# Kernel tuning notes

Measured on AMD Instinct MI355X. Metric: run time of the kernel, lower is better.

The kernel has to match this reference:

```python
import jax, jax.numpy as jnp
import numpy as np

TEMPERATURE = 0.5
EPS = 1e-8  # torch CosineSimilarity eps


def setup_inputs() -> dict:
    key = jax.random.key(0)
    k1, k2 = jax.random.split(key)
    zis = jax.random.normal(k1, (65536, 256), dtype=jnp.float32)
    zjs = jax.random.normal(k2, (65536, 256), dtype=jnp.float32)
    # default soft labels: one-hot on the positive (first) logit column
    soft_labels = jnp.zeros((4, 3), dtype=jnp.float32).at[:, 0].set(1.0)
    return {"zis": zis, "zjs": zjs, "soft_labels": soft_labels}


def reference(zis, zjs, soft_labels):
    n, d = zis.shape
    nc = n // 2  # number of chunks of size 2
    zi = zis.reshape(nc, 2, d)
    zj = zjs.reshape(nc, 2, d)
    reps = jnp.concatenate([zj, zi], axis=1)  # (nc, 4, d) = cat([zjs, zis])
    # cosine similarity with eps clamp as in torch.nn.CosineSimilarity
    norm = jnp.maximum(jnp.linalg.norm(reps, axis=-1, keepdims=True), EPS)
    reps_n = reps / norm
    sim = jnp.einsum('nid,njd->nij', reps_n, reps_n)  # (nc, 4, 4)
    # positives: diag(sim, +2) then diag(sim, -2) -> cols [2,3,0,1]
    pos = sim[:, jnp.arange(4), jnp.array([2, 3, 0, 1])]  # (nc, 4)
    # negatives: mask removes main diag and +-2 diagonals -> 2 cols per row
    neg_idx = jnp.array([[1, 3], [0, 2], [1, 3], [0, 2]])  # (4, 2)
    neg = jnp.take_along_axis(sim, neg_idx[None, :, :], axis=2)  # (nc, 4, 2)
    logits = jnp.concatenate([pos[..., None], neg], axis=-1) / TEMPERATURE  # (nc,4,3)
    # criterion: exp-normalize (softmax) then -(log ps * soft_labels).sum()
    logp = jax.nn.log_softmax(logits, axis=-1)
    loss = -(logp * soft_labels[None, :, :]).sum()
    return loss / (2 * n)
```

## Files before the change

### kernel.cpp

```cpp
#include <hip/hip_runtime.h>
#include <math.h>


constexpr int D = 256;

__device__ __forceinline__ float dot4(float4 a, float4 b) {
    return fmaf(a.x, b.x, fmaf(a.y, b.y, fmaf(a.z, b.z, a.w * b.w)));
}

template <int CTRL>
__device__ __forceinline__ float dpp_add(float x) {
    int y = __builtin_amdgcn_update_dpp(0, __float_as_int(x), CTRL, 0xF, 0xF, true);
    return x + __int_as_float(y);
}

__device__ __forceinline__ float red16(float x) {
    x = dpp_add<0xB1>(x);
    x = dpp_add<0x4E>(x);
    x = dpp_add<0x124>(x);
    x = dpp_add<0x128>(x);
    return x;
}

__device__ __forceinline__ float rowloss(float a, float b, float c,
                                         float s0, float s1, float s2) {
    float m = fmaxf(fmaxf(a, b), c);
    float lse = m + __logf(__expf(a - m) + __expf(b - m) + __expf(c - m));
    return s0 * (lse - a) + s1 * (lse - b) + s2 * (lse - c);
}

__global__ __launch_bounds__(256, 4) void ntxent_stage1(
    const float* __restrict__ zis, const float* __restrict__ zjs,
    const float* __restrict__ sl, float* __restrict__ partial, int nc) {
    const int lane = threadIdx.x & 63;
    const int wid  = threadIdx.x >> 6;
    const int t    = lane & 15;
    const int q    = lane >> 4;

    const int gwave = blockIdx.x * 4 + wid;
    const int nwave = gridDim.x * 4;
    const int nquad = (nc + 3) >> 2;

    const float sl00 = sl[0],  sl01 = sl[1],  sl02 = sl[2];
    const float sl10 = sl[3],  sl11 = sl[4],  sl12 = sl[5];
    const float sl20 = sl[6],  sl21 = sl[7],  sl22 = sl[8];
    const float sl30 = sl[9],  sl31 = sl[10], sl32 = sl[11];

    float wsum = 0.0f;
    for (int quad = gwave; quad < nquad; quad += nwave) {
        const int g = quad * 4 + q;
        const bool valid = g < nc;
        const int gc = valid ? g : 0;

        const float* rj = zjs + (size_t)(2 * gc) * D;
        const float* ri = zis + (size_t)(2 * gc) * D;
        const int o = t * 4;

        float4 v[16];
#pragma unroll
        for (int c = 0; c < 4; ++c) {
            v[c]      = *(const float4*)(rj + c * 64 + o);
            v[4 + c]  = *(const float4*)(rj + D + c * 64 + o);
            v[8 + c]  = *(const float4*)(ri + c * 64 + o);
            v[12 + c] = *(const float4*)(ri + D + c * 64 + o);
        }

        float n0 = 0, n1 = 0, n2 = 0, n3 = 0;
        float d01 = 0, d02 = 0, d03 = 0, d12 = 0, d13 = 0, d23 = 0;
#pragma unroll
        for (int c = 0; c < 4; ++c) {
            const float4 a = v[c], b = v[4 + c], cc = v[8 + c], d = v[12 + c];
            n0 += dot4(a, a);   n1 += dot4(b, b);
            n2 += dot4(cc, cc); n3 += dot4(d, d);
            d01 += dot4(a, b);  d02 += dot4(a, cc);
            d03 += dot4(a, d);  d12 += dot4(b, cc);
            d13 += dot4(b, d);  d23 += dot4(cc, d);
        }

        n0 = red16(n0);  n1 = red16(n1);  n2 = red16(n2);  n3 = red16(n3);
        d01 = red16(d01); d02 = red16(d02); d03 = red16(d03);
        d12 = red16(d12); d13 = red16(d13); d23 = red16(d23);

        const float i0 = 1.0f / fmaxf(sqrtf(n0), 1e-8f);
        const float i1 = 1.0f / fmaxf(sqrtf(n1), 1e-8f);
        const float i2 = 1.0f / fmaxf(sqrtf(n2), 1e-8f);
        const float i3 = 1.0f / fmaxf(sqrtf(n3), 1e-8f);

        const float s01 = 2.0f * d01 * i0 * i1;
        const float s02 = 2.0f * d02 * i0 * i2;
        const float s03 = 2.0f * d03 * i0 * i3;
        const float s12 = 2.0f * d12 * i1 * i2;
        const float s13 = 2.0f * d13 * i1 * i3;
        const float s23 = 2.0f * d23 * i2 * i3;

        float gl = 0.0f;
        gl += rowloss(s02, s01, s03, sl00, sl01, sl02);
        gl += rowloss(s13, s01, s12, sl10, sl11, sl12);
        gl += rowloss(s02, s12, s23, sl20, sl21, sl22);
        gl += rowloss(s13, s03, s23, sl30, sl31, sl32);
        if (valid) wsum += gl;
    }
    wsum *= 0.0625f;

#pragma unroll
    for (int off = 1; off < 64; off <<= 1) wsum += __shfl_xor(wsum, off);

    __shared__ float smem[4];
    if (lane == 0) smem[wid] = wsum;
    __syncthreads();
    if (threadIdx.x == 0)
        partial[blockIdx.x] = smem[0] + smem[1] + smem[2] + smem[3];
}

__global__ __launch_bounds__(256) void ntxent_stage2(
    const float* __restrict__ partial, int nparts, double inv_div,
    float* __restrict__ out) {
    double acc = 0.0;
    for (int i = threadIdx.x; i < nparts; i += 256) acc += (double)partial[i];
#pragma unroll
    for (int off = 1; off < 64; off <<= 1) acc += __shfl_xor(acc, off);
    __shared__ double sm[4];
    const int wid = threadIdx.x >> 6;
    if ((threadIdx.x & 63) == 0) sm[wid] = acc;
    __syncthreads();
    if (threadIdx.x == 0) out[0] = (float)((sm[0] + sm[1] + sm[2] + sm[3]) * inv_div);
}

extern "C" void kernel_launch(void* const* d_in, const int* in_sizes, int n_in,
                              void* d_out, int out_size, void* d_ws, size_t ws_size,
                              hipStream_t stream) {
    const float* zis = (const float*)d_in[0];
    const float* zjs = (const float*)d_in[1];
    const float* sl  = (const float*)d_in[2];
    float* out = (float*)d_out;
    float* partial = (float*)d_ws;

    const int n  = in_sizes[0] / D;
    const int nc = n / 2;

    const int blocks = 2048;
    ntxent_stage1<<<blocks, 256, 0, stream>>>(zis, zjs, sl, partial, nc);

    const double inv_div = 1.0 / (2.0 * (double)n);
    ntxent_stage2<<<1, 256, 0, stream>>>(partial, blocks, inv_div, out);
}
```

Measured before the change: 147.1 us.

## Double-buffer quad loads in registers and shrink grid to persistent blocks

The per-wave loop now ping-pongs between two register buffers, issuing the global loads for the next quad before computing the current one so memory latency overlaps arithmetic. The grid drops from 2048 to 512 blocks so each wave handles more quads, and launch bounds fall from 4 to 3 blocks per SIMD to leave room for the doubled register footprint. The cost is higher VGPR pressure and lower occupancy, which may reduce the latency hiding that came from running more waves at once. It also risks under-filling the device with too few blocks.

```diff
diff --git a/kernel.cpp b/kernel.cpp
--- a/kernel.cpp
+++ b/kernel.cpp
@@ -29,76 +29,104 @@
     return s0 * (lse - a) + s1 * (lse - b) + s2 * (lse - c);
 }
 
-__global__ __launch_bounds__(256, 4) void ntxent_stage1(
+__device__ __forceinline__ void load_quad(float4 v[16],
+                                          const float* __restrict__ zis,
+                                          const float* __restrict__ zjs,
+                                          int gc, int o) {
+    const float* rj = zjs + (size_t)(2 * gc) * D;
+    const float* ri = zis + (size_t)(2 * gc) * D;
+#pragma unroll
+    for (int c = 0; c < 4; ++c) {
+        v[c]      = *(const float4*)(rj + c * 64 + o);
+        v[4 + c]  = *(const float4*)(rj + D + c * 64 + o);
+        v[8 + c]  = *(const float4*)(ri + c * 64 + o);
+        v[12 + c] = *(const float4*)(ri + D + c * 64 + o);
+    }
+}
+
+struct SL { float s[12]; };
+
+__device__ __forceinline__ float compute_quad(const float4 v[16], bool valid,
+                                              const SL& L) {
+    float n0 = 0, n1 = 0, n2 = 0, n3 = 0;
+    float d01 = 0, d02 = 0, d03 = 0, d12 = 0, d13 = 0, d23 = 0;
+#pragma unroll
+    for (int c = 0; c < 4; ++c) {
+        const float4 a = v[c], b = v[4 + c], cc = v[8 + c], d = v[12 + c];
+        n0 += dot4(a, a);   n1 += dot4(b, b);
+        n2 += dot4(cc, cc); n3 += dot4(d, d);
+        d01 += dot4(a, b);  d02 += dot4(a, cc);
+        d03 += dot4(a, d);  d12 += dot4(b, cc);
+        d13 += dot4(b, d);  d23 += dot4(cc, d);
+    }
+    n0 = red16(n0);  n1 = red16(n1);  n2 = red16(n2);  n3 = red16(n3);
+    d01 = red16(d01); d02 = red16(d02); d03 = red16(d03);
+    d12 = red16(d12); d13 = red16(d13); d23 = red16(d23);
+
+    const float i0 = 1.0f / fmaxf(sqrtf(n0), 1e-8f);
+    const float i1 = 1.0f / fmaxf(sqrtf(n1), 1e-8f);
+    const float i2 = 1.0f / fmaxf(sqrtf(n2), 1e-8f);
+    const float i3 = 1.0f / fmaxf(sqrtf(n3), 1e-8f);
+
+    const float s01 = 2.0f * d01 * i0 * i1;
+    const float s02 = 2.0f * d02 * i0 * i2;
+    const float s03 = 2.0f * d03 * i0 * i3;
+    const float s12 = 2.0f * d12 * i1 * i2;
+    const float s13 = 2.0f * d13 * i1 * i3;
+    const float s23 = 2.0f * d23 * i2 * i3;
+
+    float gl = 0.0f;
+    gl += rowloss(s02, s01, s03, L.s[0], L.s[1], L.s[2]);
+    gl += rowloss(s13, s01, s12, L.s[3], L.s[4], L.s[5]);
+    gl += rowloss(s02, s12, s23, L.s[6], L.s[7], L.s[8]);
+    gl += rowloss(s13, s03, s23, L.s[9], L.s[10], L.s[11]);
+    return valid ? gl : 0.0f;
+}
+
+__global__ __launch_bounds__(256, 3) void ntxent_stage1(
     const float* __restrict__ zis, const float* __restrict__ zjs,
     const float* __restrict__ sl, float* __restrict__ partial, int nc) {
     const int lane = threadIdx.x & 63;
     const int wid  = threadIdx.x >> 6;
     const int t    = lane & 15;
     const int q    = lane >> 4;
+    const int o    = t * 4;
 
     const int gwave = blockIdx.x * 4 + wid;
     const int nwave = gridDim.x * 4;
     const int nquad = (nc + 3) >> 2;
 
-    const float sl00 = sl[0],  sl01 = sl[1],  sl02 = sl[2];
-    const float sl10 = sl[3],  sl11 = sl[4],  sl12 = sl[5];
-    const float sl20 = sl[6],  sl21 = sl[7],  sl22 = sl[8];
-    const float sl30 = sl[9],  sl31 = sl[10], sl32 = sl[11];
+    SL L;
+#pragma unroll
+    for (int i = 0; i < 12; ++i) L.s[i] = sl[i];
 
     float wsum = 0.0f;
-    for (int quad = gwave; quad < nquad; quad += nwave) {
-        const int g = quad * 4 + q;
-        const bool valid = g < nc;
-        const int gc = valid ? g : 0;
+    float4 vA[16], vB[16];
 
-        const float* rj = zjs + (size_t)(2 * gc) * D;
-        const float* ri = zis + (size_t)(2 * gc) * D;
-        const int o = t * 4;
+    int quad = gwave;
+    if (quad < nquad) {
+        {
+            const int g = quad * 4 + q;
+            load_quad(vA, zis, zjs, (g < nc) ? g : 0, o);
+        }
+        while (true) {
+            const int qB = quad + nwave;
+            if (qB < nquad) {
+                const int g = qB * 4 + q;
+                load_quad(vB, zis, zjs, (g < nc) ? g : 0, o);
+            }
+            wsum += compute_quad(vA, (quad * 4 + q) < nc, L);
+            if (qB >= nquad) break;
 
-        float4 v[16];
-#pragma unroll
-        for (int c = 0; c < 4; ++c) {
-            v[c]      = *(const float4*)(rj + c * 64 + o);
-            v[4 + c]  = *(const float4*)(rj + D + c * 64 + o);
-            v[8 + c]  = *(const float4*)(ri + c * 64 + o);
-            v[12 + c] = *(const float4*)(ri + D + c * 64 + o);
+            const int qA = qB + nwave;
+            if (qA < nquad) {
+                const int g = qA * 4 + q;
+                load_quad(vA, zis, zjs, (g < nc) ? g : 0, o);
+            }
+            wsum += compute_quad(vB, (qB * 4 + q) < nc, L);
+            if (qA >= nquad) break;
+            quad = qA;
         }
-
-        float n0 = 0, n1 = 0, n2 = 0, n3 = 0;
-        float d01 = 0, d02 = 0, d03 = 0, d12 = 0, d13 = 0, d23 = 0;
-#pragma unroll
-        for (int c = 0; c < 4; ++c) {
-            const float4 a = v[c], b = v[4 + c], cc = v[8 + c], d = v[12 + c];
-            n0 += dot4(a, a);   n1 += dot4(b, b);
-            n2 += dot4(cc, cc); n3 += dot4(d, d);
-            d01 += dot4(a, b);  d02 += dot4(a, cc);
-            d03 += dot4(a, d);  d12 += dot4(b, cc);
-            d13 += dot4(b, d);  d23 += dot4(cc, d);
-        }
-
-        n0 = red16(n0);  n1 = red16(n1);  n2 = red16(n2);  n3 = red16(n3);
-        d01 = red16(d01); d02 = red16(d02); d03 = red16(d03);
-        d12 = red16(d12); d13 = red16(d13); d23 = red16(d23);
-
-        const float i0 = 1.0f / fmaxf(sqrtf(n0), 1e-8f);
-        const float i1 = 1.0f / fmaxf(sqrtf(n1), 1e-8f);
-        const float i2 = 1.0f / fmaxf(sqrtf(n2), 1e-8f);
-        const float i3 = 1.0f / fmaxf(sqrtf(n3), 1e-8f);
-
-        const float s01 = 2.0f * d01 * i0 * i1;
-        const float s02 = 2.0f * d02 * i0 * i2;
-        const float s03 = 2.0f * d03 * i0 * i3;
-        const float s12 = 2.0f * d12 * i1 * i2;
-        const float s13 = 2.0f * d13 * i1 * i3;
-        const float s23 = 2.0f * d23 * i2 * i3;
-
-        float gl = 0.0f;
-        gl += rowloss(s02, s01, s03, sl00, sl01, sl02);
-        gl += rowloss(s13, s01, s12, sl10, sl11, sl12);
-        gl += rowloss(s02, s12, s23, sl20, sl21, sl22);
-        gl += rowloss(s13, s03, s23, sl30, sl31, sl32);
-        if (valid) wsum += gl;
     }
     wsum *= 0.0625f;
 
@@ -138,7 +166,7 @@
     const int n  = in_sizes[0] / D;
     const int nc = n / 2;
 
-    const int blocks = 2048;
+    const int blocks = 512;
     ntxent_stage1<<<blocks, 256, 0, stream>>>(zis, zjs, sl, partial, nc);
 
     const double inv_div = 1.0 / (2.0 * (double)n);
```

Result: slower. 182.3 us (+23.9%).

## Software-pipeline row loads with double buffering and shrink grid to persistent waves

Applied to the files above, without the earlier changes.

Restructures the per-wave loop into a double-buffered pipeline: it loads the second half of the current chunk group and the first half of the next while computing on the previous buffer. The grid is reduced so each wave processes several quads, and invalid tail groups clamp to the last chunk. This aims to hide global-load latency across iterations. The cost is fewer resident waves and more register pressure.

```diff
diff --git a/kernel.cpp b/kernel.cpp
--- a/kernel.cpp
+++ b/kernel.cpp
@@ -29,6 +29,34 @@
     return s0 * (lse - a) + s1 * (lse - b) + s2 * (lse - c);
 }
 
+#define LOAD8(P, G, H)                                             \
+    {                                                              \
+        const float* _rj = zjs + (size_t)(2 * (G)) * D + (H)*128 + o; \
+        const float* _ri = zis + (size_t)(2 * (G)) * D + (H)*128 + o; \
+        P##0 = *(const float4*)(_rj);                              \
+        P##1 = *(const float4*)(_rj + 64);                         \
+        P##2 = *(const float4*)(_rj + D);                          \
+        P##3 = *(const float4*)(_rj + D + 64);                     \
+        P##4 = *(const float4*)(_ri);                              \
+        P##5 = *(const float4*)(_ri + 64);                         \
+        P##6 = *(const float4*)(_ri + D);                          \
+        P##7 = *(const float4*)(_ri + D + 64);                     \
+    }
+
+#define ACC8(P)                                                    \
+    {                                                              \
+        n0  += dot4(P##0, P##0) + dot4(P##1, P##1);                \
+        n1  += dot4(P##2, P##2) + dot4(P##3, P##3);                \
+        n2  += dot4(P##4, P##4) + dot4(P##5, P##5);                \
+        n3  += dot4(P##6, P##6) + dot4(P##7, P##7);                \
+        d01 += dot4(P##0, P##2) + dot4(P##1, P##3);                \
+        d02 += dot4(P##0, P##4) + dot4(P##1, P##5);                \
+        d03 += dot4(P##0, P##6) + dot4(P##1, P##7);                \
+        d12 += dot4(P##2, P##4) + dot4(P##3, P##5);                \
+        d13 += dot4(P##2, P##6) + dot4(P##3, P##7);                \
+        d23 += dot4(P##4, P##6) + dot4(P##5, P##7);                \
+    }
+
 __global__ __launch_bounds__(256, 4) void ntxent_stage1(
     const float* __restrict__ zis, const float* __restrict__ zjs,
     const float* __restrict__ sl, float* __restrict__ partial, int nc) {
@@ -36,6 +64,7 @@
     const int wid  = threadIdx.x >> 6;
     const int t    = lane & 15;
     const int q    = lane >> 4;
+    const int o    = t * 4;
 
     const int gwave = blockIdx.x * 4 + wid;
     const int nwave = gridDim.x * 4;
@@ -47,58 +76,63 @@
     const float sl30 = sl[9],  sl31 = sl[10], sl32 = sl[11];
 
     float wsum = 0.0f;
-    for (int quad = gwave; quad < nquad; quad += nwave) {
-        const int g = quad * 4 + q;
-        const bool valid = g < nc;
-        const int gc = valid ? g : 0;
 
-        const float* rj = zjs + (size_t)(2 * gc) * D;
-        const float* ri = zis + (size_t)(2 * gc) * D;
-        const int o = t * 4;
-
-        float4 v[16];
-#pragma unroll
-        for (int c = 0; c < 4; ++c) {
-            v[c]      = *(const float4*)(rj + c * 64 + o);
-            v[4 + c]  = *(const float4*)(rj + D + c * 64 + o);
-            v[8 + c]  = *(const float4*)(ri + c * 64 + o);
-            v[12 + c] = *(const float4*)(ri + D + c * 64 + o);
-        }
-
+    if (gwave < nquad) {
+        float4 A0, A1, A2, A3, A4, A5, A6, A7;
+        float4 B0, B1, B2, B3, B4, B5, B6, B7;
         float n0 = 0, n1 = 0, n2 = 0, n3 = 0;
         float d01 = 0, d02 = 0, d03 = 0, d12 = 0, d13 = 0, d23 = 0;
-#pragma unroll
-        for (int c = 0; c < 4; ++c) {
-            const float4 a = v[c], b = v[4 + c], cc = v[8 + c], d = v[12 + c];
-            n0 += dot4(a, a);   n1 += dot4(b, b);
-            n2 += dot4(cc, cc); n3 += dot4(d, d);
-            d01 += dot4(a, b);  d02 += dot4(a, cc);
-            d03 += dot4(a, d);  d12 += dot4(b, cc);
-            d13 += dot4(b, d);  d23 += dot4(cc, d);
+
+        int k = gwave;
+        int g = k * 4 + q;
+        bool valid = g < nc;
+        int gc = valid ? g : (nc - 1);
+
+        LOAD8(A, gc, 0);
+        while (true) {
+            LOAD8(B, gc, 1);
+            ACC8(A);
+
+            const int kn = k + nwave;
+            const bool more = kn < nquad;
+            const int gn = kn * 4 + q;
+            const bool validn = more && (gn < nc);
+            const int gcn = more ? (validn ? gn : (nc - 1)) : gc;
+
+            LOAD8(A, gcn, 0);
+            ACC8(B);
+
+            {
+                float r0 = red16(n0), r1 = red16(n1), r2 = red16(n2), r3 = red16(n3);
+                float e01 = red16(d01), e02 = red16(d02), e03 = red16(d03);
+                float e12 = red16(d12), e13 = red16(d13), e23 = red16(d23);
+
+                const float i0 = 1.0f / fmaxf(sqrtf(r0), 1e-8f);
+                const float i1 = 1.0f / fmaxf(sqrtf(r1), 1e-8f);
+                const float i2 = 1.0f / fmaxf(sqrtf(r2), 1e-8f);
+                const float i3 = 1.0f / fmaxf(sqrtf(r3), 1e-8f);
+
+                const float s01 = 2.0f * e01 * i0 * i1;
+                const float s02 = 2.0f * e02 * i0 * i2;
+                const float s03 = 2.0f * e03 * i0 * i3;
+                const float s12 = 2.0f * e12 * i1 * i2;
+                const float s13 = 2.0f * e13 * i1 * i3;
+                const float s23 = 2.0f * e23 * i2 * i3;
+
+                float gl = 0.0f;
+                gl += rowloss(s02, s01, s03, sl00, sl01, sl02);
+                gl += rowloss(s13, s01, s12, sl10, sl11, sl12);
+                gl += rowloss(s02, s12, s23, sl20, sl21, sl22);
+                gl += rowloss(s13, s03, s23, sl30, sl31, sl32);
+                wsum += valid ? gl : 0.0f;
+
+                n0 = n1 = n2 = n3 = 0.0f;
+                d01 = d02 = d03 = d12 = d13 = d23 = 0.0f;
+            }
+
+            if (!more) break;
+            k = kn; gc = gcn; valid = validn;
         }
-
-        n0 = red16(n0);  n1 = red16(n1);  n2 = red16(n2);  n3 = red16(n3);
-        d01 = red16(d01); d02 = red16(d02); d03 = red16(d03);
-        d12 = red16(d12); d13 = red16(d13); d23 = red16(d23);
-
-        const float i0 = 1.0f / fmaxf(sqrtf(n0), 1e-8f);
-        const float i1 = 1.0f / fmaxf(sqrtf(n1), 1e-8f);
-        const float i2 = 1.0f / fmaxf(sqrtf(n2), 1e-8f);
-        const float i3 = 1.0f / fmaxf(sqrtf(n3), 1e-8f);
-
-        const float s01 = 2.0f * d01 * i0 * i1;
-        const float s02 = 2.0f * d02 * i0 * i2;
-        const float s03 = 2.0f * d03 * i0 * i3;
-        const float s12 = 2.0f * d12 * i1 * i2;
-        const float s13 = 2.0f * d13 * i1 * i3;
-        const float s23 = 2.0f * d23 * i2 * i3;
-
-        float gl = 0.0f;
-        gl += rowloss(s02, s01, s03, sl00, sl01, sl02);
-        gl += rowloss(s13, s01, s12, sl10, sl11, sl12);
-        gl += rowloss(s02, s12, s23, sl20, sl21, sl22);
-        gl += rowloss(s13, s03, s23, sl30, sl31, sl32);
-        if (valid) wsum += gl;
     }
     wsum *= 0.0625f;
 
@@ -138,7 +172,7 @@
     const int n  = in_sizes[0] / D;
     const int nc = n / 2;
 
-    const int blocks = 2048;
+    const int blocks = 512;
     ntxent_stage1<<<blocks, 256, 0, stream>>>(zis, zjs, sl, partial, nc);
 
     const double inv_div = 1.0 / (2.0 * (double)n);
```

Result: no change. 147.1 us (-0.0%).

## Double-buffer input tiles into LDS via async global_load_lds per wave

Applied to the files above, without the earlier changes.

Replaces the direct-to-register loads with a per-wave double-buffered pipeline that uses global_load_lds to stage the next 4-row tile of each input into LDS while the current tile is computed. Each wave now handles two chunks per iteration, with 32 lanes per chunk, and reductions are widened to 32 lanes using an extra shuffle. Blocks become single-wave (64 threads, 16KB LDS) and the grid grows, which removes the block-level shared-memory reduction. The goal is to hide HBM latency in a bandwidth-bound kernel. The cost is LDS round-trips, explicit vmcnt wait bookkeeping, and lower per-block occupancy.

```diff
diff --git a/kernel.cpp b/kernel.cpp
--- a/kernel.cpp
+++ b/kernel.cpp
@@ -14,11 +14,12 @@
     return x + __int_as_float(y);
 }
 
-__device__ __forceinline__ float red16(float x) {
+__device__ __forceinline__ float red32(float x) {
     x = dpp_add<0xB1>(x);
     x = dpp_add<0x4E>(x);
     x = dpp_add<0x124>(x);
     x = dpp_add<0x128>(x);
+    x += __shfl_xor(x, 16);
     return x;
 }
 
@@ -29,87 +30,112 @@
     return s0 * (lse - a) + s1 * (lse - b) + s2 * (lse - c);
 }
 
-__global__ __launch_bounds__(256, 4) void ntxent_stage1(
+#define AS1(p) ((const __attribute__((address_space(1))) void*)(p))
+#define AS3(p) ((__attribute__((address_space(3))) void*)(p))
+
+__device__ __forceinline__ void stage_tile(const float* __restrict__ zjs,
+                                           const float* __restrict__ zis,
+                                           int k, char* buf, int lane) {
+    const float* sj = zjs + (size_t)k * (4 * D) + lane * 4;
+    const float* si = zis + (size_t)k * (4 * D) + lane * 4;
+#pragma unroll
+    for (int i = 0; i < 4; ++i)
+        __builtin_amdgcn_global_load_lds(AS1(sj + i * D), AS3(buf + i * 1024), 16, 0, 0);
+#pragma unroll
+    for (int i = 0; i < 4; ++i)
+        __builtin_amdgcn_global_load_lds(AS1(si + i * D), AS3(buf + 4096 + i * 1024), 16, 0, 0);
+}
+
+__global__ __launch_bounds__(64, 2) void ntxent_stage1(
     const float* __restrict__ zis, const float* __restrict__ zjs,
     const float* __restrict__ sl, float* __restrict__ partial, int nc) {
-    const int lane = threadIdx.x & 63;
-    const int wid  = threadIdx.x >> 6;
-    const int t    = lane & 15;
-    const int q    = lane >> 4;
+    extern __shared__ __align__(16) char lds[];
+    const int lane = threadIdx.x;
+    const int h = lane >> 5;
+    const int t = lane & 31;
 
-    const int gwave = blockIdx.x * 4 + wid;
-    const int nwave = gridDim.x * 4;
-    const int nquad = (nc + 3) >> 2;
+    const int wave  = blockIdx.x;
+    const int nwave = gridDim.x;
+    const int ntile = (nc + 1) >> 1;
 
-    const float sl00 = sl[0],  sl01 = sl[1],  sl02 = sl[2];
-    const float sl10 = sl[3],  sl11 = sl[4],  sl12 = sl[5];
-    const float sl20 = sl[6],  sl21 = sl[7],  sl22 = sl[8];
-    const float sl30 = sl[9],  sl31 = sl[10], sl32 = sl[11];
+    float L0 = sl[0],  L1 = sl[1],  L2 = sl[2];
+    float L3 = sl[3],  L4 = sl[4],  L5 = sl[5];
+    float L6 = sl[6],  L7 = sl[7],  L8 = sl[8];
+    float L9 = sl[9],  L10 = sl[10], L11 = sl[11];
 
     float wsum = 0.0f;
-    for (int quad = gwave; quad < nquad; quad += nwave) {
-        const int g = quad * 4 + q;
-        const bool valid = g < nc;
-        const int gc = valid ? g : 0;
+    int k = wave;
+    if (k < ntile) {
+        stage_tile(zjs, zis, k, lds, lane);
+        int cur = 0;
+        while (true) {
+            const int kn = k + nwave;
+            const bool more = kn < ntile;
+            if (more) {
+                stage_tile(zjs, zis, kn, lds + (cur ^ 1) * 8192, lane);
+                asm volatile("s_waitcnt vmcnt(8)" ::: "memory");
+            } else {
+                asm volatile("s_waitcnt vmcnt(0)" ::: "memory");
+            }
 
-        const float* rj = zjs + (size_t)(2 * gc) * D;
-        const float* ri = zis + (size_t)(2 * gc) * D;
-        const int o = t * 4;
+            {
+                const float4* bp = (const float4*)(lds + cur * 8192);
+                const int r0 = (2 * h) * 64;
+                const int r1 = r0 + 64;
+                const int r2 = 256 + r0;
+                const int r3 = r2 + 64;
+                float4 a0 = bp[r0 + t], a1 = bp[r0 + 32 + t];
+                float4 b0 = bp[r1 + t], b1 = bp[r1 + 32 + t];
+                float4 c0 = bp[r2 + t], c1 = bp[r2 + 32 + t];
+                float4 e0 = bp[r3 + t], e1 = bp[r3 + 32 + t];
 
-        float4 v[16];
-#pragma unroll
-        for (int c = 0; c < 4; ++c) {
-            v[c]      = *(const float4*)(rj + c * 64 + o);
-            v[4 + c]  = *(const float4*)(rj + D + c * 64 + o);
-            v[8 + c]  = *(const float4*)(ri + c * 64 + o);
-            v[12 + c] = *(const float4*)(ri + D + c * 64 + o);
+                float n0 = dot4(a0, a0) + dot4(a1, a1);
+                float n1 = dot4(b0, b0) + dot4(b1, b1);
+                float n2 = dot4(c0, c0) + dot4(c1, c1);
+                float n3 = dot4(e0, e0) + dot4(e1, e1);
+                float d01 = dot4(a0, b0) + dot4(a1, b1);
+                float d02 = dot4(a0, c0) + dot4(a1, c1);
+                float d03 = dot4(a0, e0) + dot4(a1, e1);
+                float d12 = dot4(b0, c0) + dot4(b1, c1);
+                float d13 = dot4(b0, e0) + dot4(b1, e1);
+                float d23 = dot4(c0, e0) + dot4(c1, e1);
+
+                n0 = red32(n0);  n1 = red32(n1);  n2 = red32(n2);  n3 = red32(n3);
+                d01 = red32(d01); d02 = red32(d02); d03 = red32(d03);
+                d12 = red32(d12); d13 = red32(d13); d23 = red32(d23);
+
+                const float i0 = 1.0f / fmaxf(sqrtf(n0), 1e-8f);
+                const float i1 = 1.0f / fmaxf(sqrtf(n1), 1e-8f);
+                const float i2 = 1.0f / fmaxf(sqrtf(n2), 1e-8f);
+                const float i3 = 1.0f / fmaxf(sqrtf(n3), 1e-8f);
+
+                const float s01 = 2.0f * d01 * i0 * i1;
+                const float s02 = 2.0f * d02 * i0 * i2;
+                const float s03 = 2.0f * d03 * i0 * i3;
+                const float s12 = 2.0f * d12 * i1 * i2;
+                const float s13 = 2.0f * d13 * i1 * i3;
+                const float s23 = 2.0f * d23 * i2 * i3;
+
+                float gl = 0.0f;
+                gl += rowloss(s02, s01, s03, L0, L1, L2);
+                gl += rowloss(s13, s01, s12, L3, L4, L5);
+                gl += rowloss(s02, s12, s23, L6, L7, L8);
+                gl += rowloss(s13, s03, s23, L9, L10, L11);
+
+                const bool valid = (2 * k + h) < nc;
+                wsum += valid ? gl : 0.0f;
+            }
+
+            if (!more) break;
+            k = kn;
+            cur ^= 1;
         }
-
-        float n0 = 0, n1 = 0, n2 = 0, n3 = 0;
-        float d01 = 0, d02 = 0, d03 = 0, d12 = 0, d13 = 0, d23 = 0;
-#pragma unroll
-        for (int c = 0; c < 4; ++c) {
-            const float4 a = v[c], b = v[4 + c], cc = v[8 + c], d = v[12 + c];
-            n0 += dot4(a, a);   n1 += dot4(b, b);
-            n2 += dot4(cc, cc); n3 += dot4(d, d);
-            d01 += dot4(a, b);  d02 += dot4(a, cc);
-            d03 += dot4(a, d);  d12 += dot4(b, cc);
-            d13 += dot4(b, d);  d23 += dot4(cc, d);
-        }
-
-        n0 = red16(n0);  n1 = red16(n1);  n2 = red16(n2);  n3 = red16(n3);
-        d01 = red16(d01); d02 = red16(d02); d03 = red16(d03);
-        d12 = red16(d12); d13 = red16(d13); d23 = red16(d23);
-
-        const float i0 = 1.0f / fmaxf(sqrtf(n0), 1e-8f);
-        const float i1 = 1.0f / fmaxf(sqrtf(n1), 1e-8f);
-        const float i2 = 1.0f / fmaxf(sqrtf(n2), 1e-8f);
-        const float i3 = 1.0f / fmaxf(sqrtf(n3), 1e-8f);
-
-        const float s01 = 2.0f * d01 * i0 * i1;
-        const float s02 = 2.0f * d02 * i0 * i2;
-        const float s03 = 2.0f * d03 * i0 * i3;
-        const float s12 = 2.0f * d12 * i1 * i2;
-        const float s13 = 2.0f * d13 * i1 * i3;
-        const float s23 = 2.0f * d23 * i2 * i3;
-
-        float gl = 0.0f;
-        gl += rowloss(s02, s01, s03, sl00, sl01, sl02);
-        gl += rowloss(s13, s01, s12, sl10, sl11, sl12);
-        gl += rowloss(s02, s12, s23, sl20, sl21, sl22);
-        gl += rowloss(s13, s03, s23, sl30, sl31, sl32);
-        if (valid) wsum += gl;
     }
-    wsum *= 0.0625f;
+    wsum *= (1.0f / 32.0f);
 
 #pragma unroll
     for (int off = 1; off < 64; off <<= 1) wsum += __shfl_xor(wsum, off);
-
-    __shared__ float smem[4];
-    if (lane == 0) smem[wid] = wsum;
-    __syncthreads();
-    if (threadIdx.x == 0)
-        partial[blockIdx.x] = smem[0] + smem[1] + smem[2] + smem[3];
+    if (lane == 0) partial[blockIdx.x] = wsum;
 }
 
 __global__ __launch_bounds__(256) void ntxent_stage2(
@@ -138,8 +164,8 @@
     const int n  = in_sizes[0] / D;
     const int nc = n / 2;
 
-    const int blocks = 2048;
-    ntxent_stage1<<<blocks, 256, 0, stream>>>(zis, zjs, sl, partial, nc);
+    const int blocks = 2560;
+    ntxent_stage1<<<blocks, 64, 16384, stream>>>(zis, zjs, sl, partial, nc);
 
     const double inv_div = 1.0 / (2.0 * (double)n);
     ntxent_stage2<<<1, 256, 0, stream>>>(partial, blocks, inv_div, out);
```

Result: slower. 154.7 us (+5.1%).
